# Kernel tuning notes

Measured on AMD Instinct MI355X. Metric: run time of the kernel, lower is better.

## Reference

```python
import jax, jax.numpy as jnp
import numpy as np

N_HEAD = 16
HEAD_DIM = 64
ROPE_BASE = 10000.0


def _rope_cos_sin(T, dim, dtype):
    inv_freq = 1.0 / (ROPE_BASE ** (np.arange(0, dim, 2, dtype=np.float32) / dim))
    t = np.arange(T, dtype=np.float32)
    freqs = np.outer(t, inv_freq)              # [T, dim/2]
    emb = np.concatenate([freqs, freqs], -1)   # [T, dim]
    return jnp.asarray(np.cos(emb), dtype), jnp.asarray(np.sin(emb), dtype)


def _rotate_half(x):
    x1, x2 = x[..., : x.shape[-1] // 2], x[..., x.shape[-1] // 2 :]
    return jnp.concatenate([-x2, x1], axis=-1)


def setup_inputs() -> dict:
    key = jax.random.key(0)
    k1, k2, k3 = jax.random.split(key, 3)
    B, T, C = 4, 2048, 1024
    x = jax.random.normal(k1, (B, T, C), jnp.float32)
    w_qkv = jax.random.normal(k2, (C, 3 * C), jnp.float32) * (C ** -0.5)
    w_proj = jax.random.normal(k3, (C, C), jnp.float32) * (C ** -0.5)
    return {"x": x, "w_qkv": w_qkv, "w_proj": w_proj}


def reference(x, w_qkv, w_proj):
    B, T, C = x.shape
    H, D = N_HEAD, HEAD_DIM
    qkv = x @ w_qkv                                   # [B, T, 3C]
    q, k, v = jnp.split(qkv, 3, axis=-1)
    # [B, H, T, D]
    q = q.reshape(B, T, H, D).transpose(0, 2, 1, 3)
    k = k.reshape(B, T, H, D).transpose(0, 2, 1, 3)
    v = v.reshape(B, T, H, D).transpose(0, 2, 1, 3)
    cos, sin = _rope_cos_sin(T, D, x.dtype)           # [T, D]
    q = q * cos + _rotate_half(q) * sin
    k = k * cos + _rotate_half(k) * sin
    scale = D ** -0.5
    scores = jnp.einsum("bhqd,bhkd->bhqk", q, k) * scale
    causal = jnp.tril(jnp.ones((T, T), bool))
    scores = jnp.where(causal, scores, jnp.finfo(scores.dtype).min)
    attn = jax.nn.softmax(scores, axis=-1)
    y = jnp.einsum("bhqk,bhkd->bhqd", attn, v)        # [B, H, T, D]
    y = y.transpose(0, 2, 1, 3).reshape(B, T, C)
    return y @ w_proj
```

## Files before the change

kernel.cpp:

```cpp
#include <hip/hip_runtime.h>
#include <cstdint>

typedef unsigned short u16;
typedef __attribute__((ext_vector_type(4))) float f32x4;
typedef __attribute__((ext_vector_type(4))) unsigned short u16x4;
typedef __attribute__((ext_vector_type(8))) unsigned short u16x8;
typedef __attribute__((ext_vector_type(8))) __bf16 bf16x8;

#define DEV __device__ __forceinline__

DEV u16 f2bf(float f) {
  union { float f; uint32_t u; } x{f};
  uint32_t r = (x.u + 0x7fffu + ((x.u >> 16) & 1u)) >> 16;
  return (u16)r;
}

DEV void gl_lds16(const void* g, void* l) {
  __builtin_amdgcn_global_load_lds((__attribute__((address_space(1))) void*)(g),
                                   (__attribute__((address_space(3))) void*)(l),
                                   16, 0, 0);
}

__global__ __launch_bounds__(256) void cast_f2b(const float* __restrict__ in,
                                                u16* __restrict__ out) {
  int i = blockIdx.x * 256 + threadIdx.x;
  float4 v = ((const float4*)in)[i];
  u16x4 o = { f2bf(v.x), f2bf(v.y), f2bf(v.z), f2bf(v.w) };
  ((u16x4*)out)[i] = o;
}

__global__ __launch_bounds__(256) void transpose_cast(const float* __restrict__ in,
                                                      u16* __restrict__ out, int R, int C) {
  __shared__ float tile[64][65];
  const int c0 = blockIdx.x * 64, r0 = blockIdx.y * 64;
  const int tx = threadIdx.x & 63, ty = threadIdx.x >> 6;
  for (int r = ty; r < 64; r += 4) tile[r][tx] = in[(size_t)(r0 + r) * C + c0 + tx];
  __syncthreads();
  for (int r = ty; r < 64; r += 4) out[(size_t)(c0 + r) * R + r0 + tx] = f2bf(tile[tx][r]);
}

template <int EPI>
__global__ __launch_bounds__(256) void gemm_bt(const u16* __restrict__ A,
                                               const u16* __restrict__ Bt,
                                               u16* __restrict__ qo, u16* __restrict__ ko,
                                               u16* __restrict__ vo, float* __restrict__ outf) {
  extern __shared__ char lds_occupancy_pad[];
  const int K = 1024;
  __shared__ __align__(16) u16 As[128 * 64];
  __shared__ __align__(16) u16 Bs[128 * 64];
  const int m0 = blockIdx.y * 128, n0 = blockIdx.x * 128;
  const int tid = threadIdx.x;
  const int w = tid >> 6, lane = tid & 63, quad = lane >> 4, l15 = lane & 15;
  const int mw = (w >> 1) * 64, nw = (w & 1) * 64;

  const int srow = tid >> 3;
  const int schunk = ((tid & 7) ^ (srow & 7)) * 8;

  f32x4 acc[4][4];
#pragma unroll
  for (int i = 0; i < 4; ++i)
#pragma unroll
    for (int j = 0; j < 4; ++j) acc[i][j] = f32x4{0.f, 0.f, 0.f, 0.f};

  const u16* ga0 = A + (size_t)(m0 + srow) * K + schunk;
  const u16* gb0 = Bt + (size_t)(n0 + srow) * K + schunk;

  const int sw7 = l15 & 7;
  int aoff[4], boff[4];
#pragma unroll
  for (int i = 0; i < 4; ++i) aoff[i] = (mw + i * 16 + l15) * 64;
#pragma unroll
  for (int j = 0; j < 4; ++j) boff[j] = (nw + j * 16 + l15) * 64;
  int coff[2];
#pragma unroll
  for (int kk = 0; kk < 2; ++kk) coff[kk] = ((kk * 4 + quad) ^ sw7) * 8;

  for (int k0 = 0; k0 < K; k0 += 64) {
#pragma unroll
    for (int ss = 0; ss < 4; ++ss) {
      gl_lds16(ga0 + (size_t)ss * 32 * K + k0, As + ss * 2048 + tid * 8);
      gl_lds16(gb0 + (size_t)ss * 32 * K + k0, Bs + ss * 2048 + tid * 8);
    }
    __syncthreads();
#pragma unroll
    for (int kk = 0; kk < 2; ++kk) {
      bf16x8 af[4], bfv[4];
#pragma unroll
      for (int i = 0; i < 4; ++i) af[i] = *(const bf16x8*)(As + aoff[i] + coff[kk]);
#pragma unroll
      for (int j = 0; j < 4; ++j) bfv[j] = *(const bf16x8*)(Bs + boff[j] + coff[kk]);
#pragma unroll
      for (int i = 0; i < 4; ++i)
#pragma unroll
        for (int j = 0; j < 4; ++j)
          acc[i][j] = __builtin_amdgcn_mfma_f32_16x16x32_bf16(af[i], bfv[j], acc[i][j], 0, 0, 0);
    }
    __syncthreads();
  }

  if (EPI == 1) {
#pragma unroll
    for (int i = 0; i < 4; ++i)
#pragma unroll
      for (int j = 0; j < 4; ++j)
#pragma unroll
        for (int r = 0; r < 4; ++r) {
          int row = m0 + mw + i * 16 + quad * 4 + r;
          int col = n0 + nw + j * 16 + l15;
          outf[(size_t)row * 1024 + col] = acc[i][j][r];
        }
    return;
  }
  const int s = n0 >> 10;
  const int hh = ((n0 & 1023) + nw) >> 6;
  if (s == 2) {
#pragma unroll
    for (int i = 0; i < 4; ++i)
#pragma unroll
      for (int r = 0; r < 4; ++r) {
        int row = m0 + mw + i * 16 + quad * 4 + r;
        int b = row >> 11, t = row & 2047;
        size_t base = ((size_t)(b * 16 + hh) * 2048 + t) * 64;
#pragma unroll
        for (int j = 0; j < 4; ++j) vo[base + j * 16 + l15] = f2bf(acc[i][j][r]);
      }
  } else {
    u16* dst = (s == 0) ? qo : ko;
    const float QS = (s == 0) ? 0.18033688011112042f : 1.0f;
    const float C1 = -0.4152410118609203f;
    const float R2PI = 0.15915494309189535f;
    const float inv0 = __builtin_amdgcn_exp2f((float)l15 * C1) * R2PI;
    const float inv1 = __builtin_amdgcn_exp2f((float)(16 + l15) * C1) * R2PI;
#pragma unroll
    for (int i = 0; i < 4; ++i)
#pragma unroll
      for (int r = 0; r < 4; ++r) {
        int row = m0 + mw + i * 16 + quad * 4 + r;
        int b = row >> 11, t = row & 2047;
        size_t base = ((size_t)(b * 16 + hh) * 2048 + t) * 64;
        float tf = (float)t;
        float a0 = tf * inv0; a0 -= floorf(a0);
        float a1 = tf * inv1; a1 -= floorf(a1);
        float c0 = __builtin_amdgcn_cosf(a0), s0 = __builtin_amdgcn_sinf(a0);
        float c1 = __builtin_amdgcn_cosf(a1), s1 = __builtin_amdgcn_sinf(a1);
        float x0 = acc[i][0][r], y0 = acc[i][2][r];
        float x1 = acc[i][1][r], y1 = acc[i][3][r];
        dst[base + l15]      = f2bf((x0 * c0 - y0 * s0) * QS);
        dst[base + 32 + l15] = f2bf((y0 * c0 + x0 * s0) * QS);
        dst[base + 16 + l15] = f2bf((x1 * c1 - y1 * s1) * QS);
        dst[base + 48 + l15] = f2bf((y1 * c1 + x1 * s1) * QS);
      }
  }
}

__global__ __launch_bounds__(256) void transpose_v(const u16* __restrict__ v,
                                                   u16* __restrict__ vt) {
  const int bh = blockIdx.y, t0 = blockIdx.x * 64;
  __shared__ __align__(16) u16 tile[64][72];
  const int tid = threadIdx.x;
  const int row = tid >> 3, col = (tid & 7) * 8;
#pragma unroll
  for (int rr = 0; rr < 2; ++rr) {
    int r = row + rr * 32;
    *(u16x8*)(&tile[r][col]) = *(const u16x8*)(v + ((size_t)bh * 2048 + t0 + r) * 64 + col);
  }
  __syncthreads();
#pragma unroll
  for (int rr = 0; rr < 2; ++rr) {
    int d = row + rr * 32;
    u16x8 o;
#pragma unroll
    for (int j = 0; j < 8; ++j) o[j] = tile[col + j][d];
    *(u16x8*)(vt + ((size_t)bh * 64 + d) * 2048 + t0 + col) = o;
  }
}

__global__ __launch_bounds__(256) void attn_kernel(const u16* __restrict__ q,
                                                   const u16* __restrict__ k,
                                                   const u16* __restrict__ vt,
                                                   u16* __restrict__ y) {
  const int T = 2048;
  const int bh = blockIdx.x;
  const int qi = 15 - blockIdx.y;
  const int q0 = qi * 128;
  const int tid = threadIdx.x;
  const int w = tid >> 6, lane = tid & 63, quad = lane >> 4, l15 = lane & 15;
  __shared__ __align__(16) u16 Ks[64 * 64];
  __shared__ __align__(16) u16 Vs[64 * 64];
  __shared__ __align__(16) u16 Pq[4 * 32 * 72];
  u16* Pw = Pq + w * 32 * 72;

  const int sw = l15 & 7;
  int koff[4][2], voff[4][2];
#pragma unroll
  for (int kf = 0; kf < 4; ++kf) {
    koff[kf][0] = (kf * 16 + l15) * 64 + ((quad ^ sw) * 8);
    koff[kf][1] = (kf * 16 + l15) * 64 + (((quad + 4) ^ sw) * 8);
  }
#pragma unroll
  for (int df = 0; df < 4; ++df) {
    voff[df][0] = (df * 16 + l15) * 64 + ((quad ^ sw) * 8);
    voff[df][1] = (df * 16 + l15) * 64 + (((quad + 4) ^ sw) * 8);
  }
  const int pwoff = l15 * 72 + quad * 4;
  const int proff = l15 * 72 + quad * 8;

  const int r_ = tid >> 3, c_ = tid & 7, ssw = r_ & 7;
  const u16* kg = k + (size_t)bh * T * 64;
  const u16* vg = vt + (size_t)bh * 64 * T;
  const int sk0 = r_ * 64 + (c_ ^ ssw) * 8;
  const int sk1 = (r_ + 32) * 64 + (c_ ^ ssw) * 8;
  const int sv0 = r_ * T + (c_ ^ ssw) * 8;
  const int sv1 = (r_ + 32) * T + (c_ ^ ssw) * 8;

  const int b_ = bh >> 4, h_ = bh & 15;
  const int q0w = q0 + w * 32;

  bf16x8 qf_[2][2];
#pragma unroll
  for (int qf = 0; qf < 2; ++qf)
#pragma unroll
    for (int h = 0; h < 2; ++h)
      qf_[qf][h] = *(const bf16x8*)(q + ((size_t)bh * T + q0w + qf * 16 + l15) * 64 + h * 32 + quad * 8);

  f32x4 o[2][4];
  float li[2] = {0.f, 0.f};
#pragma unroll
  for (int qf = 0; qf < 2; ++qf)
#pragma unroll
    for (int df = 0; df < 4; ++df) o[qf][df] = f32x4{0.f, 0.f, 0.f, 0.f};

  const int nit = 2 * qi + 2;

  for (int it = 0; it < nit; ++it) {
    const int kb = it * 64;
    gl_lds16(kg + (size_t)kb * 64 + sk0, Ks + tid * 8);
    gl_lds16(kg + (size_t)kb * 64 + sk1, Ks + 2048 + tid * 8);
    gl_lds16(vg + kb + sv0, Vs + tid * 8);
    gl_lds16(vg + kb + sv1, Vs + 2048 + tid * 8);
    __syncthreads();

    bf16x8 ka[4][2];
#pragma unroll
    for (int kf = 0; kf < 4; ++kf) {
      ka[kf][0] = *(const bf16x8*)(Ks + koff[kf][0]);
      ka[kf][1] = *(const bf16x8*)(Ks + koff[kf][1]);
    }
    f32x4 st[2][4];
    __builtin_amdgcn_s_setprio(1);
#pragma unroll
    for (int kf = 0; kf < 4; ++kf)
#pragma unroll
      for (int qf = 0; qf < 2; ++qf) {
        f32x4 s = f32x4{0.f, 0.f, 0.f, 0.f};
        s = __builtin_amdgcn_mfma_f32_16x16x32_bf16(ka[kf][0], qf_[qf][0], s, 0, 0, 0);
        s = __builtin_amdgcn_mfma_f32_16x16x32_bf16(ka[kf][1], qf_[qf][1], s, 0, 0, 0);
        st[qf][kf] = s;
      }
    __builtin_amdgcn_s_setprio(0);

    if (it >= nit - 2) {
#pragma unroll
      for (int qf = 0; qf < 2; ++qf) {
        const int qrow = q0w + qf * 16 + l15;
#pragma unroll
        for (int kf = 0; kf < 4; ++kf)
#pragma unroll
          for (int r = 0; r < 4; ++r)
            if (kb + kf * 16 + quad * 4 + r > qrow) st[qf][kf][r] = -__builtin_inff();
      }
    }

#pragma unroll
    for (int qf = 0; qf < 2; ++qf) {
      float rs = 0.f;
#pragma unroll
      for (int kf = 0; kf < 4; ++kf) {
        float p0 = __builtin_amdgcn_exp2f(st[qf][kf][0]);
        float p1 = __builtin_amdgcn_exp2f(st[qf][kf][1]);
        float p2 = __builtin_amdgcn_exp2f(st[qf][kf][2]);
        float p3 = __builtin_amdgcn_exp2f(st[qf][kf][3]);
        rs += (p0 + p1) + (p2 + p3);
        union { float f; uint32_t u; } u0{p0}, u1{p1}, u2{p2}, u3{p3};
        uint32_t pk01 = __builtin_amdgcn_perm(u1.u + 0x8000u, u0.u + 0x8000u, 0x07060302u);
        uint32_t pk23 = __builtin_amdgcn_perm(u3.u + 0x8000u, u2.u + 0x8000u, 0x07060302u);
        uint2 pk; pk.x = pk01; pk.y = pk23;
        *(uint2*)(Pw + qf * 16 * 72 + pwoff + kf * 16) = pk;
      }
      li[qf] += rs;
    }

#pragma unroll
    for (int qf = 0; qf < 2; ++qf) {
      bf16x8 pb0 = *(const bf16x8*)(Pw + qf * 16 * 72 + proff);
      bf16x8 pb1 = *(const bf16x8*)(Pw + qf * 16 * 72 + proff + 32);
      __builtin_amdgcn_s_setprio(1);
#pragma unroll
      for (int df = 0; df < 4; ++df) {
        bf16x8 va0 = *(const bf16x8*)(Vs + voff[df][0]);
        bf16x8 va1 = *(const bf16x8*)(Vs + voff[df][1]);
        o[qf][df] = __builtin_amdgcn_mfma_f32_16x16x32_bf16(va0, pb0, o[qf][df], 0, 0, 0);
        o[qf][df] = __builtin_amdgcn_mfma_f32_16x16x32_bf16(va1, pb1, o[qf][df], 0, 0, 0);
      }
      __builtin_amdgcn_s_setprio(0);
    }
    __syncthreads();
  }

#pragma unroll
  for (int qf = 0; qf < 2; ++qf) {
    float l = li[qf];
    l += __shfl_xor(l, 16, 64);
    l += __shfl_xor(l, 32, 64);
    const float inv = 1.f / l;
    const size_t base = ((size_t)b_ * 2048 + q0w + qf * 16 + l15) * 1024 + h_ * 64;
#pragma unroll
    for (int df = 0; df < 4; ++df) {
      u16x4 ov;
#pragma unroll
      for (int r = 0; r < 4; ++r) ov[r] = f2bf(o[qf][df][r] * inv);
      *(u16x4*)(y + base + df * 16 + quad * 4) = ov;
    }
  }
}

extern "C" void kernel_launch(void* const* d_in, const int* in_sizes, int n_in,
                              void* d_out, int out_size, void* d_ws, size_t ws_size,
                              hipStream_t stream) {
  const float* x = (const float*)d_in[0];
  const float* w_qkv = (const float*)d_in[1];
  const float* w_proj = (const float*)d_in[2];
  float* out = (float*)d_out;

  u16* xb = (u16*)d_ws;
  u16* wqkvT = xb + 8388608;
  u16* wprojT = wqkvT + 3145728;
  u16* qb = wprojT + 1048576;
  u16* kbuf = qb + 8388608;
  u16* vb = kbuf + 8388608;
  u16* vtb = vb + 8388608;
  u16* yb = xb;

  cast_f2b<<<8192, 256, 0, stream>>>(x, xb);
  transpose_cast<<<dim3(48, 16), 256, 0, stream>>>(w_qkv, wqkvT, 1024, 3072);
  transpose_cast<<<dim3(16, 16), 256, 0, stream>>>(w_proj, wprojT, 1024, 1024);
  gemm_bt<0><<<dim3(24, 64), 256, 21504, stream>>>(xb, wqkvT, qb, kbuf, vb, nullptr);
  transpose_v<<<dim3(32, 64), 256, 0, stream>>>(vb, vtb);
  attn_kernel<<<dim3(64, 16), 256, 0, stream>>>(qb, kbuf, vtb, yb);
  gemm_bt<1><<<dim3(8, 64), 256, 0, stream>>>(yb, wprojT, nullptr, nullptr, nullptr, out);
}
```

Before: 245.6 us.

## Fuse V transpose into QKV GEMM epilogue and merge prep kernels

The QKV GEMM epilogue now stages each V tile in LDS with an XOR swizzle and writes it out directly in [B,H,D,T] layout. This removes the separate transpose_v kernel and its 16 MB round trip through global memory. The three input cast/transpose kernels are also merged into one launch that dispatches on block index, which saves launch overhead. In exchange the epilogue reuses the GEMM's As/Bs LDS buffers and adds a barrier.

```diff
diff --git a/kernel.cpp b/kernel.cpp
--- a/kernel.cpp
+++ b/kernel.cpp
@@ -21,19 +21,26 @@
                                    16, 0, 0);
 }
 
-__global__ __launch_bounds__(256) void cast_f2b(const float* __restrict__ in,
-                                                u16* __restrict__ out) {
-  int i = blockIdx.x * 256 + threadIdx.x;
-  float4 v = ((const float4*)in)[i];
-  u16x4 o = { f2bf(v.x), f2bf(v.y), f2bf(v.z), f2bf(v.w) };
-  ((u16x4*)out)[i] = o;
-}
-
-__global__ __launch_bounds__(256) void transpose_cast(const float* __restrict__ in,
-                                                      u16* __restrict__ out, int R, int C) {
+__global__ __launch_bounds__(256) void prep(const float* __restrict__ x, u16* __restrict__ xb,
+                                            const float* __restrict__ wqkv, u16* __restrict__ wqkvT,
+                                            const float* __restrict__ wproj, u16* __restrict__ wprojT) {
+  const int bid = blockIdx.x, tid = threadIdx.x;
+  if (bid < 8192) {
+    int i = bid * 256 + tid;
+    float4 v = ((const float4*)x)[i];
+    u16x4 o = { f2bf(v.x), f2bf(v.y), f2bf(v.z), f2bf(v.w) };
+    ((u16x4*)xb)[i] = o;
+    return;
+  }
   __shared__ float tile[64][65];
-  const int c0 = blockIdx.x * 64, r0 = blockIdx.y * 64;
-  const int tx = threadIdx.x & 63, ty = threadIdx.x >> 6;
+  const float* in; u16* out; int R, C, bx, by;
+  if (bid < 8960) {
+    int idx = bid - 8192; in = wqkv;  out = wqkvT;  R = 1024; C = 3072; bx = idx % 48; by = idx / 48;
+  } else {
+    int idx = bid - 8960; in = wproj; out = wprojT; R = 1024; C = 1024; bx = idx & 15; by = idx >> 4;
+  }
+  const int c0 = bx * 64, r0 = by * 64;
+  const int tx = tid & 63, ty = tid >> 6;
   for (int r = ty; r < 64; r += 4) tile[r][tx] = in[(size_t)(r0 + r) * C + c0 + tx];
   __syncthreads();
   for (int r = ty; r < 64; r += 4) out[(size_t)(c0 + r) * R + r0 + tx] = f2bf(tile[tx][r]);
@@ -112,19 +119,34 @@
     return;
   }
   const int s = n0 >> 10;
-  const int hh = ((n0 & 1023) + nw) >> 6;
   if (s == 2) {
-#pragma unroll
-    for (int i = 0; i < 4; ++i)
-#pragma unroll
-      for (int r = 0; r < 4; ++r) {
-        int row = m0 + mw + i * 16 + quad * 4 + r;
-        int b = row >> 11, t = row & 2047;
-        size_t base = ((size_t)(b * 16 + hh) * 2048 + t) * 64;
-#pragma unroll
-        for (int j = 0; j < 4; ++j) vo[base + j * 16 + l15] = f2bf(acc[i][j][r]);
-      }
+    u16* tile = (w & 1) ? Bs : As;
+#pragma unroll
+    for (int j = 0; j < 4; ++j) {
+      const int d = j * 16 + l15;
+      const int swz = l15 * 8;
+#pragma unroll
+      for (int i = 0; i < 4; ++i)
+#pragma unroll
+        for (int r = 0; r < 4; ++r) {
+          int tl = mw + i * 16 + quad * 4 + r;
+          tile[d * 128 + (tl ^ swz)] = f2bf(acc[i][j][r]);
+        }
+    }
+    __syncthreads();
+    const int b = m0 >> 11, t0g = m0 & 2047;
+    const int hh0 = (n0 & 1023) >> 6;
+    const int tch = tid & 15;
+#pragma unroll
+    for (int p = 0; p < 8; ++p) {
+      int row = (tid >> 4) + p * 16;
+      int d = row & 63, head = row >> 6;
+      const u16* src = head ? Bs : As;
+      u16x8 v = *(const u16x8*)(src + d * 128 + ((tch * 8) ^ ((d & 15) * 8)));
+      *(u16x8*)(vo + ((size_t)((b * 16 + hh0 + head) * 64 + d)) * 2048 + t0g + tch * 8) = v;
+    }
   } else {
+    const int hh = ((n0 & 1023) + nw) >> 6;
     u16* dst = (s == 0) ? qo : ko;
     const float QS = (s == 0) ? 0.18033688011112042f : 1.0f;
     const float C1 = -0.4152410118609203f;
@@ -153,28 +175,6 @@
   }
 }
 
-__global__ __launch_bounds__(256) void transpose_v(const u16* __restrict__ v,
-                                                   u16* __restrict__ vt) {
-  const int bh = blockIdx.y, t0 = blockIdx.x * 64;
-  __shared__ __align__(16) u16 tile[64][72];
-  const int tid = threadIdx.x;
-  const int row = tid >> 3, col = (tid & 7) * 8;
-#pragma unroll
-  for (int rr = 0; rr < 2; ++rr) {
-    int r = row + rr * 32;
-    *(u16x8*)(&tile[r][col]) = *(const u16x8*)(v + ((size_t)bh * 2048 + t0 + r) * 64 + col);
-  }
-  __syncthreads();
-#pragma unroll
-  for (int rr = 0; rr < 2; ++rr) {
-    int d = row + rr * 32;
-    u16x8 o;
-#pragma unroll
-    for (int j = 0; j < 8; ++j) o[j] = tile[col + j][d];
-    *(u16x8*)(vt + ((size_t)bh * 64 + d) * 2048 + t0 + col) = o;
-  }
-}
-
 __global__ __launch_bounds__(256) void attn_kernel(const u16* __restrict__ q,
                                                    const u16* __restrict__ k,
                                                    const u16* __restrict__ vt,
@@ -337,15 +337,11 @@
   u16* wprojT = wqkvT + 3145728;
   u16* qb = wprojT + 1048576;
   u16* kbuf = qb + 8388608;
-  u16* vb = kbuf + 8388608;
-  u16* vtb = vb + 8388608;
+  u16* vtb = kbuf + 8388608;
   u16* yb = xb;
 
-  cast_f2b<<<8192, 256, 0, stream>>>(x, xb);
-  transpose_cast<<<dim3(48, 16), 256, 0, stream>>>(w_qkv, wqkvT, 1024, 3072);
-  transpose_cast<<<dim3(16, 16), 256, 0, stream>>>(w_proj, wprojT, 1024, 1024);
-  gemm_bt<0><<<dim3(24, 64), 256, 21504, stream>>>(xb, wqkvT, qb, kbuf, vb, nullptr);
-  transpose_v<<<dim3(32, 64), 256, 0, stream>>>(vb, vtb);
+  prep<<<9216, 256, 0, stream>>>(x, xb, w_qkv, wqkvT, w_proj, wprojT);
+  gemm_bt<0><<<dim3(24, 64), 256, 21504, stream>>>(xb, wqkvT, qb, kbuf, vtb, nullptr);
   attn_kernel<<<dim3(64, 16), 256, 0, stream>>>(qb, kbuf, vtb, yb);
   gemm_bt<1><<<dim3(8, 64), 256, 0, stream>>>(yb, wprojT, nullptr, nullptr, nullptr, out);
 }
```

Measured after the change: 233.1 us, median of 3. 5.1% less time.
